# Optimization experiments

Measured on AMD Instinct MI355X. Metric: run time of the kernel, lower is better.

Reference implementation:

```python
import jax, jax.numpy as jnp
import numpy as np

B, S, F_IN = 8, 2048, 1024
H, SC = 512, 256
N_LAYERS = 3


def _glorot(key, shape):
    fan_in, fan_out = shape[-2], shape[-1]
    lim = float(np.sqrt(6.0 / (fan_in + fan_out)))
    return jax.random.uniform(key, shape, jnp.float32, -lim, lim)


def setup_inputs() -> dict:
    key = jax.random.key(0)
    ks = jax.random.split(key, 8)
    x = jax.random.normal(ks[0], (B, S, F_IN), jnp.float32)
    Wp = _glorot(ks[1], (F_IN, H)); bp = jnp.zeros((H,), jnp.float32)
    gcn_W = _glorot(ks[2], (N_LAYERS, H, H)); gcn_b = jnp.zeros((N_LAYERS, H), jnp.float32)
    s1_W = _glorot(ks[3], (H, SC)); s1_b = jnp.zeros((SC,), jnp.float32)
    s2_W = _glorot(ks[4], (SC, SC // 2)); s2_b = jnp.zeros((SC // 2,), jnp.float32)
    s3_W = _glorot(ks[5], (SC // 2, 1)); s3_b = jnp.zeros((1,), jnp.float32)
    return {"x": x, "Wp": Wp, "bp": bp, "gcn_W": gcn_W, "gcn_b": gcn_b,
            "s1_W": s1_W, "s1_b": s1_b, "s2_W": s2_W, "s2_b": s2_b,
            "s3_W": s3_W, "s3_b": s3_b}


def _build_adj(seq_len):
    # tridiagonal band: self + immediate temporal neighbors
    a = jnp.eye(seq_len, dtype=jnp.float32)
    a = a + jnp.eye(seq_len, k=1, dtype=jnp.float32) + jnp.eye(seq_len, k=-1, dtype=jnp.float32)
    deg = a.sum(axis=1)
    dinv = jnp.power(deg + 1e-8, -0.5)
    # D^{-1/2} A D^{-1/2}
    return dinv[:, None] * a * dinv[None, :]


def reference(x, Wp, bp, gcn_W, gcn_b, s1_W, s1_b, s2_W, s2_b, s3_W, s3_b):
    seq_len = x.shape[1]
    adj = _build_adj(seq_len)  # [S, S]
    h = jnp.einsum('bsf,fh->bsh', x, Wp) + bp  # feature projection
    for i in range(N_LAYERS):
        support = jnp.einsum('bsh,hk->bsk', h, gcn_W[i])
        h = jnp.einsum('st,btk->bsk', adj, support) + gcn_b[i]
        if i < N_LAYERS - 1:
            h = jax.nn.relu(h)  # dropout is identity in eval mode
    z = jax.nn.relu(jnp.einsum('bsh,hc->bsc', h, s1_W) + s1_b)
    z = jax.nn.relu(jnp.einsum('bsc,cd->bsd', z, s2_W) + s2_b)
    scores = jax.nn.sigmoid(jnp.einsum('bsd,do->bso', z, s3_W) + s3_b)
    return scores[..., 0]  # [B, S]
```

## Files before the change

kernel.cpp:

```cpp
#include <hip/hip_runtime.h>
#include <hip/hip_fp16.h>
#include <cstdint>
#include <cstddef>


typedef _Float16 f16;
typedef _Float16 f16x8 __attribute__((ext_vector_type(8)));
typedef float    f32x4 __attribute__((ext_vector_type(4)));

__device__ __forceinline__ void async_cp16(const void* g, void* l) {
  __builtin_amdgcn_global_load_lds((const __attribute__((address_space(1))) void*)g,
                                   (__attribute__((address_space(3))) void*)l, 16, 0, 0);
}

__device__ __forceinline__ f16x8 splat8(f16 v) {
  f16x8 r;
#pragma unroll
  for (int e = 0; e < 8; ++e) r[e] = v;
  return r;
}

template<int BM, int BN, bool RELU, bool HAS_BIAS, int AMODE>
__global__ __launch_bounds__(512, 4) void gemm_f16_kernel(
    const void* __restrict__ Aptr, const f16* __restrict__ BT,
    f16* __restrict__ C, const float* __restrict__ bias,
    int M, int N, int K)
{
  constexpr int BK = 64;
  constexpr int NT = 512;
  constexpr int WAVES_M = 2, WAVES_N = 4;
  constexpr int WM = BM / WAVES_M;
  constexpr int WN = BN / WAVES_N;
  constexpr int TM = WM / 16;
  constexpr int TN = WN / 16;
  constexpr int ITER_B = (BN * BK) / (NT * 8);
  constexpr int S = 2048;
  constexpr int AROWS = (AMODE == 2) ? (BM + 2) : BM;

  __shared__ __align__(16) f16 sA[AROWS * BK];
  __shared__ __align__(16) f16 sB[BN * BK];

  const int tid  = threadIdx.x;
  const int lane = tid & 63;
  const int wave = tid >> 6;
  const int wm   = wave / WAVES_N;
  const int wn   = wave % WAVES_N;
  const int m0   = blockIdx.x * BM;
  const int n0   = blockIdx.y * BN;
  const int quad = lane >> 4;
  const int l16  = lane & 15;

  const float dM = 0.57735026919f;
  const float dE = 0.70710678118f;

  f16 cf[TM][3];
  if constexpr (AMODE == 2) {
#pragma unroll
    for (int mi = 0; mi < TM; ++mi) {
      const int grow = m0 + wm * WM + mi * 16 + l16;
      const int s = grow & (S - 1);
      const float dsv = (s == 0 || s == S - 1) ? dE : dM;
      cf[mi][0] = (f16)((s > 0)     ? dsv * ((s - 1 == 0) ? dE : dM)     : 0.0f);
      cf[mi][1] = (f16)(dsv * dsv);
      cf[mi][2] = (f16)((s < S - 1) ? dsv * ((s + 1 == S - 1) ? dE : dM) : 0.0f);
    }
  }

  uint32_t offA = 0;
  {
    const int row = tid >> 3;
    const int q   = (tid & 7) ^ (row & 7);
    if constexpr (AMODE == 1)
      offA = (uint32_t)(((size_t)(m0 + row) * K + q * 8) * 4);
  }

  f32x4 acc[TM][TN];
#pragma unroll
  for (int i = 0; i < TM; ++i)
#pragma unroll
    for (int j = 0; j < TN; ++j)
      acc[i][j] = (f32x4){0.f, 0.f, 0.f, 0.f};

  float4 pa0, pa1;
  if constexpr (AMODE == 1) {
    const char* base = (const char*)Aptr;
    const float4* p = (const float4*)(base + offA);
    pa0 = p[0]; pa1 = p[1];
  }

  for (int kt = 0; kt < K; kt += BK) {
#pragma unroll
    for (int j = 0; j < ITER_B; ++j) {
      const int linear = j * NT + tid;
      const int row = linear >> 3;
      const int q   = (linear & 7) ^ (row & 7);
      async_cp16(BT + (size_t)(n0 + row) * K + kt + q * 8, &sB[linear * 8]);
    }
    if constexpr (AMODE == 1) {
      f16x8 o;
      o[0] = (f16)pa0.x; o[1] = (f16)pa0.y; o[2] = (f16)pa0.z; o[3] = (f16)pa0.w;
      o[4] = (f16)pa1.x; o[5] = (f16)pa1.y; o[6] = (f16)pa1.z; o[7] = (f16)pa1.w;
      *(f16x8*)&sA[(size_t)tid * 8] = o;
    } else {
      {
        const int chunk = tid + 8;
        const int row = chunk >> 3;
        const int q   = (chunk & 7) ^ (row & 7);
        async_cp16((const f16*)Aptr + (size_t)(m0 + row - 1) * K + kt + q * 8,
                   &sA[chunk * 8]);
      }
      if (tid < 16) {
        const int hi = tid >> 3;
        const int ldsrow = hi ? (BM + 1) : 0;
        const int i = tid & 7;
        const int q = i ^ (ldsrow & 7);
        int g = m0 - 1 + ldsrow;
        g = g < 0 ? 0 : (g >= M ? M - 1 : g);
        f16x8 v = *(const f16x8*)((const f16*)Aptr + (size_t)g * K + kt + q * 8);
        *(f16x8*)&sA[(size_t)(ldsrow * 8 + i) * 8] = v;
      }
    }
    __syncthreads();

    if constexpr (AMODE == 1) {
      if (kt + BK < K) {
        const char* base = (const char*)Aptr + (size_t)(kt + BK) * 4;
        const float4* p = (const float4*)(base + offA);
        pa0 = p[0]; pa1 = p[1];
      }
    }

#pragma unroll
    for (int kk = 0; kk < 2; ++kk) {
      const int c = quad + kk * 4;
      f16x8 af[TM], bf[TN];
#pragma unroll
      for (int mi = 0; mi < TM; ++mi) {
        if constexpr (AMODE == 2) {
          const int ldr = wm * WM + mi * 16 + l16 + 1;
          f16x8 pv = *(const f16x8*)&sA[(ldr - 1) * 64 + ((c ^ ((ldr - 1) & 7)) * 8)];
          f16x8 sv = *(const f16x8*)&sA[(ldr    ) * 64 + ((c ^ ((ldr    ) & 7)) * 8)];
          f16x8 nv = *(const f16x8*)&sA[(ldr + 1) * 64 + ((c ^ ((ldr + 1) & 7)) * 8)];
          f16x8 r = pv * splat8(cf[mi][0]);
          r += sv * splat8(cf[mi][1]);
          r += nv * splat8(cf[mi][2]);
          af[mi] = r;
        } else {
          const int ml = wm * WM + mi * 16 + l16;
          af[mi] = *(const f16x8*)&sA[ml * 64 + ((c ^ (ml & 7)) * 8)];
        }
      }
#pragma unroll
      for (int ni = 0; ni < TN; ++ni) {
        const int nl = wn * WN + ni * 16 + l16;
        bf[ni] = *(const f16x8*)&sB[nl * 64 + ((c ^ (nl & 7)) * 8)];
      }
#pragma unroll
      for (int mi = 0; mi < TM; ++mi)
#pragma unroll
        for (int ni = 0; ni < TN; ++ni)
          acc[mi][ni] = __builtin_amdgcn_mfma_f32_16x16x32_f16(
              af[mi], bf[ni], acc[mi][ni], 0, 0, 0);
    }
    __syncthreads();
  }

#pragma unroll
  for (int ni = 0; ni < TN; ++ni) {
    const int nc = n0 + wn * WN + ni * 16 + l16;
    const float bv = HAS_BIAS ? bias[nc] : 0.0f;
#pragma unroll
    for (int mi = 0; mi < TM; ++mi) {
#pragma unroll
      for (int r = 0; r < 4; ++r) {
        const int mr = m0 + wm * WM + mi * 16 + quad * 4 + r;
        float v = acc[mi][ni][r] + bv;
        if (RELU) v = fmaxf(v, 0.0f);
        C[(size_t)mr * N + nc] = (f16)v;
      }
    }
  }
}

__global__ __launch_bounds__(256) void head_fused_kernel(
    const f16* __restrict__ h, const f16* __restrict__ S1T,
    const f16* __restrict__ S2T,
    const float* __restrict__ s1b, const float* __restrict__ s2b,
    const float* __restrict__ s3w, const float* __restrict__ s3b,
    float* __restrict__ out)
{
  __shared__ __align__(16) char smem[36864 + 32 * 264 * 2];
  f16* sA  = (f16*)smem;
  f16* sB  = (f16*)(smem + 4096);
  f16* zs  = (f16*)(smem + 36864);
  f16* z2s = (f16*)smem;
  f16* sB2 = (f16*)(smem + 8704);

  const int tid  = threadIdx.x;
  const int lane = tid & 63;
  const int wave = tid >> 6;
  const int quad = lane >> 4;
  const int l16  = lane & 15;
  const int m0   = blockIdx.x * 32;

  f32x4 acc[2][4];
#pragma unroll
  for (int i = 0; i < 2; ++i)
#pragma unroll
    for (int j = 0; j < 4; ++j) acc[i][j] = (f32x4){0.f, 0.f, 0.f, 0.f};

  for (int kt = 0; kt < 512; kt += 64) {
    __syncthreads();
    {
      const int linear = tid;
      const int row = linear >> 3;
      const int q   = (linear & 7) ^ (row & 7);
      async_cp16(h + (size_t)(m0 + row) * 512 + kt + q * 8, &sA[linear * 8]);
    }
#pragma unroll
    for (int j = 0; j < 8; ++j) {
      const int linear = j * 256 + tid;
      const int row = linear >> 3;
      const int q   = (linear & 7) ^ (row & 7);
      async_cp16(S1T + (size_t)row * 512 + kt + q * 8, &sB[linear * 8]);
    }
    __syncthreads();
#pragma unroll
    for (int kk = 0; kk < 2; ++kk) {
      const int c = quad + kk * 4;
      f16x8 af[2], bf[4];
#pragma unroll
      for (int mi = 0; mi < 2; ++mi) {
        const int ml = mi * 16 + l16;
        af[mi] = *(const f16x8*)&sA[ml * 64 + ((c ^ (ml & 7)) * 8)];
      }
#pragma unroll
      for (int ni = 0; ni < 4; ++ni) {
        const int nl = wave * 64 + ni * 16 + l16;
        bf[ni] = *(const f16x8*)&sB[nl * 64 + ((c ^ (nl & 7)) * 8)];
      }
#pragma unroll
      for (int mi = 0; mi < 2; ++mi)
#pragma unroll
        for (int ni = 0; ni < 4; ++ni)
          acc[mi][ni] = __builtin_amdgcn_mfma_f32_16x16x32_f16(
              af[mi], bf[ni], acc[mi][ni], 0, 0, 0);
    }
  }
#pragma unroll
  for (int ni = 0; ni < 4; ++ni) {
    const int nc = wave * 64 + ni * 16 + l16;
    const float bv = s1b[nc];
#pragma unroll
    for (int mi = 0; mi < 2; ++mi)
#pragma unroll
      for (int r = 0; r < 4; ++r) {
        const int row = mi * 16 + quad * 4 + r;
        zs[row * 264 + nc] = (f16)fmaxf(acc[mi][ni][r] + bv, 0.0f);
      }
  }
  __syncthreads();

  f32x4 acc2[2][2];
#pragma unroll
  for (int i = 0; i < 2; ++i)
#pragma unroll
    for (int j = 0; j < 2; ++j) acc2[i][j] = (f32x4){0.f, 0.f, 0.f, 0.f};

  for (int kt2 = 0; kt2 < 4; ++kt2) {
    __syncthreads();
#pragma unroll
    for (int j = 0; j < 4; ++j) {
      const int linear = j * 256 + tid;
      const int row = linear >> 3;
      const int q   = (linear & 7) ^ (row & 7);
      async_cp16(S2T + (size_t)row * 256 + kt2 * 64 + q * 8, &sB2[linear * 8]);
    }
    __syncthreads();
#pragma unroll
    for (int kk = 0; kk < 2; ++kk) {
      const int c = quad + kk * 4;
      f16x8 af[2], bf[2];
#pragma unroll
      for (int mi = 0; mi < 2; ++mi) {
        const int row = mi * 16 + l16;
        af[mi] = *(const f16x8*)&zs[row * 264 + (kt2 * 8 + c) * 8];
      }
#pragma unroll
      for (int ni = 0; ni < 2; ++ni) {
        const int nl = wave * 32 + ni * 16 + l16;
        bf[ni] = *(const f16x8*)&sB2[nl * 64 + ((c ^ (nl & 7)) * 8)];
      }
#pragma unroll
      for (int mi = 0; mi < 2; ++mi)
#pragma unroll
        for (int ni = 0; ni < 2; ++ni)
          acc2[mi][ni] = __builtin_amdgcn_mfma_f32_16x16x32_f16(
              af[mi], bf[ni], acc2[mi][ni], 0, 0, 0);
    }
  }
  __syncthreads();
#pragma unroll
  for (int ni = 0; ni < 2; ++ni) {
    const int nc = wave * 32 + ni * 16 + l16;
    const float bv = s2b[nc];
#pragma unroll
    for (int mi = 0; mi < 2; ++mi)
#pragma unroll
      for (int r = 0; r < 4; ++r) {
        const int row = mi * 16 + quad * 4 + r;
        z2s[row * 136 + nc] = (f16)fmaxf(acc2[mi][ni][r] + bv, 0.0f);
      }
  }
  __syncthreads();

  const int m  = tid >> 3;
  const int qd = tid & 7;
  float p = 0.f;
#pragma unroll
  for (int j = 0; j < 2; ++j) {
    f16x8 v = *(const f16x8*)&z2s[m * 136 + qd * 16 + j * 8];
#pragma unroll
    for (int e = 0; e < 8; ++e) p += (float)v[e] * s3w[qd * 16 + j * 8 + e];
  }
  p += __shfl_xor(p, 1);
  p += __shfl_xor(p, 2);
  p += __shfl_xor(p, 4);
  if (qd == 0) out[m0 + m] = 1.0f / (1.0f + expf(-(p + s3b[0])));
}

__global__ __launch_bounds__(256) void prep_kernel(
    const float* __restrict__ Wp, f16* __restrict__ WpT,
    const float* __restrict__ gW, f16* __restrict__ GT,
    const float* __restrict__ s1W, f16* __restrict__ S1T,
    const float* __restrict__ s2W, f16* __restrict__ S2T)
{
  __shared__ f16 s[64 * 68];
  const int tid = threadIdx.x;
  int b = blockIdx.x;

  const float* W; f16* WT; int K, N, tile;
  if (b < 128)      { W = Wp;  WT = WpT; K = 1024; N = 512; tile = b; }
  else if (b < 320) { const int i = (b - 128) >> 6;
                      W = gW + (size_t)i * 262144; WT = GT + (size_t)i * 262144;
                      K = 512; N = 512; tile = (b - 128) & 63; }
  else if (b < 352) { W = s1W; WT = S1T; K = 512; N = 256; tile = b - 320; }
  else              { W = s2W; WT = S2T; K = 256; N = 128; tile = b - 352; }

  const int nt = tile % (N >> 6);
  const int kt = tile / (N >> 6);
#pragma unroll
  for (int it = 0; it < 16; ++it) {
    const int i  = it * 256 + tid;
    const int rk = i >> 6, rn = i & 63;
    s[rn * 68 + rk] = (f16)W[(size_t)(kt * 64 + rk) * N + nt * 64 + rn];
  }
  __syncthreads();
#pragma unroll
  for (int it = 0; it < 16; ++it) {
    const int i  = it * 256 + tid;
    const int rn = i >> 6, rk = i & 63;
    WT[(size_t)(nt * 64 + rn) * K + kt * 64 + rk] = s[rn * 68 + rk];
  }
}

extern "C" void kernel_launch(void* const* d_in, const int* in_sizes, int n_in,
                              void* d_out, int out_size, void* d_ws, size_t ws_size,
                              hipStream_t stream) {
  (void)in_sizes; (void)n_in; (void)out_size; (void)ws_size;
  const float* x   = (const float*)d_in[0];
  const float* Wp  = (const float*)d_in[1];
  const float* bp  = (const float*)d_in[2];
  const float* gW  = (const float*)d_in[3];
  const float* gb  = (const float*)d_in[4];
  const float* s1W = (const float*)d_in[5];
  const float* s1b = (const float*)d_in[6];
  const float* s2W = (const float*)d_in[7];
  const float* s2b = (const float*)d_in[8];
  const float* s3W = (const float*)d_in[9];
  const float* s3b = (const float*)d_in[10];
  float* out = (float*)d_out;

  constexpr int M = 16384;
  char* ws = (char*)d_ws;
  f16* hA  = (f16*)(ws + 0);
  f16* hB  = (f16*)(ws + 16777216);
  f16* WpT = (f16*)(ws + 33554432);
  f16* GT  = (f16*)(ws + 34603008);
  f16* S1T = (f16*)(ws + 36175872);
  f16* S2T = (f16*)(ws + 36438016);

  prep_kernel<<<360, 256, 0, stream>>>(Wp, WpT, gW, GT, s1W, S1T, s2W, S2T);

  gemm_f16_kernel<64, 256, false, true, 1>
      <<<dim3(M / 64, 2), 512, 0, stream>>>(x, WpT, hA, bp, M, 512, 1024);

  gemm_f16_kernel<64, 256, true, true, 2>
      <<<dim3(M / 64, 2), 512, 0, stream>>>(hA, GT, hB, gb, M, 512, 512);
  gemm_f16_kernel<64, 256, true, true, 2>
      <<<dim3(M / 64, 2), 512, 0, stream>>>(hB, GT + 262144, hA, gb + 512, M, 512, 512);
  gemm_f16_kernel<64, 256, false, true, 2>
      <<<dim3(M / 64, 2), 512, 0, stream>>>(hA, GT + 524288, hB, gb + 1024, M, 512, 512);

  head_fused_kernel<<<M / 32, 256, 0, stream>>>(hB, S1T, S2T, s1b, s2b, s3W, s3b, out);
}
```

Measured before the change: 198.2 us.

## Fuse three GCN layers into one kernel with LDS-resident activations and halo recompute

Replaces the three per-layer GEMM launches with one kernel. Each block loads a 96-row tile of h (64 output rows plus 16-row halos on each side) into LDS and runs all three layers in place, applying the tridiagonal stencil on the fly. This removes the global write and re-read of the intermediate activations between layers and two kernel launches. In exchange it recomputes the halo rows (1.5x the GEMM work), uses about 128KB of LDS so only one block fits per CU, and streams weights in small unpipelined K-steps with a barrier each step.

```diff
diff --git a/kernel.cpp b/kernel.cpp
--- a/kernel.cpp
+++ b/kernel.cpp
@@ -20,24 +20,22 @@
   return r;
 }
 
-template<int BM, int BN, bool RELU, bool HAS_BIAS, int AMODE>
-__global__ __launch_bounds__(512, 4) void gemm_f16_kernel(
-    const void* __restrict__ Aptr, const f16* __restrict__ BT,
+template<int BM, int BN, bool RELU, bool HAS_BIAS>
+__global__ __launch_bounds__(512, 4) void proj_gemm_kernel(
+    const float* __restrict__ Aptr, const f16* __restrict__ BT,
     f16* __restrict__ C, const float* __restrict__ bias,
     int M, int N, int K)
 {
   constexpr int BK = 64;
   constexpr int NT = 512;
-  constexpr int WAVES_M = 2, WAVES_N = 4;
-  constexpr int WM = BM / WAVES_M;
+  constexpr int WAVES_N = 4;
+  constexpr int WM = BM / 2;
   constexpr int WN = BN / WAVES_N;
   constexpr int TM = WM / 16;
   constexpr int TN = WN / 16;
   constexpr int ITER_B = (BN * BK) / (NT * 8);
-  constexpr int S = 2048;
-  constexpr int AROWS = (AMODE == 2) ? (BM + 2) : BM;
-
-  __shared__ __align__(16) f16 sA[AROWS * BK];
+
+  __shared__ __align__(16) f16 sA[BM * BK];
   __shared__ __align__(16) f16 sB[BN * BK];
 
   const int tid  = threadIdx.x;
@@ -50,28 +48,11 @@
   const int quad = lane >> 4;
   const int l16  = lane & 15;
 
-  const float dM = 0.57735026919f;
-  const float dE = 0.70710678118f;
-
-  f16 cf[TM][3];
-  if constexpr (AMODE == 2) {
-#pragma unroll
-    for (int mi = 0; mi < TM; ++mi) {
-      const int grow = m0 + wm * WM + mi * 16 + l16;
-      const int s = grow & (S - 1);
-      const float dsv = (s == 0 || s == S - 1) ? dE : dM;
-      cf[mi][0] = (f16)((s > 0)     ? dsv * ((s - 1 == 0) ? dE : dM)     : 0.0f);
-      cf[mi][1] = (f16)(dsv * dsv);
-      cf[mi][2] = (f16)((s < S - 1) ? dsv * ((s + 1 == S - 1) ? dE : dM) : 0.0f);
-    }
-  }
-
-  uint32_t offA = 0;
+  uint32_t offA;
   {
     const int row = tid >> 3;
     const int q   = (tid & 7) ^ (row & 7);
-    if constexpr (AMODE == 1)
-      offA = (uint32_t)(((size_t)(m0 + row) * K + q * 8) * 4);
+    offA = (uint32_t)(((size_t)(m0 + row) * K + q * 8) * 4);
   }
 
   f32x4 acc[TM][TN];
@@ -82,9 +63,8 @@
       acc[i][j] = (f32x4){0.f, 0.f, 0.f, 0.f};
 
   float4 pa0, pa1;
-  if constexpr (AMODE == 1) {
-    const char* base = (const char*)Aptr;
-    const float4* p = (const float4*)(base + offA);
+  {
+    const float4* p = (const float4*)((const char*)Aptr + offA);
     pa0 = p[0]; pa1 = p[1];
   }
 
@@ -96,38 +76,17 @@
       const int q   = (linear & 7) ^ (row & 7);
       async_cp16(BT + (size_t)(n0 + row) * K + kt + q * 8, &sB[linear * 8]);
     }
-    if constexpr (AMODE == 1) {
+    {
       f16x8 o;
       o[0] = (f16)pa0.x; o[1] = (f16)pa0.y; o[2] = (f16)pa0.z; o[3] = (f16)pa0.w;
       o[4] = (f16)pa1.x; o[5] = (f16)pa1.y; o[6] = (f16)pa1.z; o[7] = (f16)pa1.w;
       *(f16x8*)&sA[(size_t)tid * 8] = o;
-    } else {
-      {
-        const int chunk = tid + 8;
-        const int row = chunk >> 3;
-        const int q   = (chunk & 7) ^ (row & 7);
-        async_cp16((const f16*)Aptr + (size_t)(m0 + row - 1) * K + kt + q * 8,
-                   &sA[chunk * 8]);
-      }
-      if (tid < 16) {
-        const int hi = tid >> 3;
-        const int ldsrow = hi ? (BM + 1) : 0;
-        const int i = tid & 7;
-        const int q = i ^ (ldsrow & 7);
-        int g = m0 - 1 + ldsrow;
-        g = g < 0 ? 0 : (g >= M ? M - 1 : g);
-        f16x8 v = *(const f16x8*)((const f16*)Aptr + (size_t)g * K + kt + q * 8);
-        *(f16x8*)&sA[(size_t)(ldsrow * 8 + i) * 8] = v;
-      }
-    }
-    __syncthreads();
-
-    if constexpr (AMODE == 1) {
-      if (kt + BK < K) {
-        const char* base = (const char*)Aptr + (size_t)(kt + BK) * 4;
-        const float4* p = (const float4*)(base + offA);
-        pa0 = p[0]; pa1 = p[1];
-      }
+    }
+    __syncthreads();
+
+    if (kt + BK < K) {
+      const float4* p = (const float4*)((const char*)Aptr + (size_t)(kt + BK) * 4 + offA);
+      pa0 = p[0]; pa1 = p[1];
     }
 
 #pragma unroll
@@ -136,19 +95,8 @@
       f16x8 af[TM], bf[TN];
 #pragma unroll
       for (int mi = 0; mi < TM; ++mi) {
-        if constexpr (AMODE == 2) {
-          const int ldr = wm * WM + mi * 16 + l16 + 1;
-          f16x8 pv = *(const f16x8*)&sA[(ldr - 1) * 64 + ((c ^ ((ldr - 1) & 7)) * 8)];
-          f16x8 sv = *(const f16x8*)&sA[(ldr    ) * 64 + ((c ^ ((ldr    ) & 7)) * 8)];
-          f16x8 nv = *(const f16x8*)&sA[(ldr + 1) * 64 + ((c ^ ((ldr + 1) & 7)) * 8)];
-          f16x8 r = pv * splat8(cf[mi][0]);
-          r += sv * splat8(cf[mi][1]);
-          r += nv * splat8(cf[mi][2]);
-          af[mi] = r;
-        } else {
-          const int ml = wm * WM + mi * 16 + l16;
-          af[mi] = *(const f16x8*)&sA[ml * 64 + ((c ^ (ml & 7)) * 8)];
-        }
+        const int ml = wm * WM + mi * 16 + l16;
+        af[mi] = *(const f16x8*)&sA[ml * 64 + ((c ^ (ml & 7)) * 8)];
       }
 #pragma unroll
       for (int ni = 0; ni < TN; ++ni) {
@@ -177,6 +125,143 @@
         float v = acc[mi][ni][r] + bv;
         if (RELU) v = fmaxf(v, 0.0f);
         C[(size_t)mr * N + nc] = (f16)v;
+      }
+    }
+  }
+}
+
+__global__ __launch_bounds__(512, 2) void gcn_fused_kernel(
+    const f16* __restrict__ hin, const f16* __restrict__ GT,
+    const float* __restrict__ gb, f16* __restrict__ hout, int M)
+{
+  constexpr int ROWS = 96, HALO = 16, BK = 32, S = 2048;
+  constexpr int H = 512;
+  constexpr int TM = 3, TN = 8;
+
+  __shared__ __align__(16) f16 sh[ROWS * H];
+  __shared__ __align__(16) f16 sW[H * BK];
+
+  const int tid  = threadIdx.x;
+  const int lane = tid & 63;
+  const int wave = tid >> 6;
+  const int wm   = wave >> 2;
+  const int wn   = wave & 3;
+  const int quad = lane >> 4;
+  const int l16  = lane & 15;
+  const int m0   = blockIdx.x * 64;
+
+  const float dM = 0.57735026919f;
+  const float dE = 0.70710678118f;
+
+  f16 cf[TM][3];
+  int rS[TM], rP[TM], rN[TM];
+#pragma unroll
+  for (int mi = 0; mi < TM; ++mi) {
+    const int lr = wm * 48 + mi * 16 + l16;
+    const int g  = m0 - HALO + lr;
+    const int s  = g & (S - 1);
+    const float dsv = (s == 0 || s == S - 1) ? dE : dM;
+    cf[mi][0] = (f16)((s > 0)     ? dsv * ((s - 1 == 0) ? dE : dM)     : 0.0f);
+    cf[mi][1] = (f16)(dsv * dsv);
+    cf[mi][2] = (f16)((s < S - 1) ? dsv * ((s + 1 == S - 1) ? dE : dM) : 0.0f);
+    rS[mi] = lr;
+    rP[mi] = (lr > 0)        ? lr - 1 : 0;
+    rN[mi] = (lr < ROWS - 1) ? lr + 1 : ROWS-1;
+  }
+
+#pragma unroll
+  for (int j = 0; j < 12; ++j) {
+    const int row = j * 8 + wave;
+    const int q   = lane ^ (row & 7) ^ (lane & ~63);
+    const int cin = lane;
+    const int qq  = cin ^ (row & 7);
+    int g = m0 - HALO + row;
+    g = g < 0 ? 0 : (g >= M ? M - 1 : g);
+    (void)q;
+    async_cp16(hin + (size_t)g * H + qq * 8, &sh[((size_t)j * 512 + tid) * 8]);
+  }
+
+  for (int L = 0; L < 3; ++L) {
+    const f16* WL = GT + (size_t)L * 262144;
+    const float* bL = gb + L * 512;
+
+    f32x4 acc[TM][TN];
+#pragma unroll
+    for (int i = 0; i < TM; ++i)
+#pragma unroll
+      for (int j = 0; j < TN; ++j)
+        acc[i][j] = (f32x4){0.f, 0.f, 0.f, 0.f};
+
+    for (int kt = 0; kt < H; kt += BK) {
+#pragma unroll
+      for (int j = 0; j < 4; ++j) {
+        const int linear = j * 512 + tid;
+        const int row = linear >> 2;
+        const int cin = linear & 3;
+        const int qq  = cin ^ (row & 3);
+        async_cp16(WL + (size_t)row * H + kt + qq * 8, &sW[(size_t)linear * 8]);
+      }
+      __syncthreads();
+
+      const int cb = kt >> 3;
+      f16x8 af[TM], bf[TN];
+#pragma unroll
+      for (int mi = 0; mi < TM; ++mi) {
+        const int c = cb + quad;
+        f16x8 pv = *(const f16x8*)&sh[rP[mi] * H + ((c ^ (rP[mi] & 7)) * 8)];
+        f16x8 sv = *(const f16x8*)&sh[rS[mi] * H + ((c ^ (rS[mi] & 7)) * 8)];
+        f16x8 nv = *(const f16x8*)&sh[rN[mi] * H + ((c ^ (rN[mi] & 7)) * 8)];
+        f16x8 r = pv * splat8(cf[mi][0]);
+        r += sv * splat8(cf[mi][1]);
+        r += nv * splat8(cf[mi][2]);
+        af[mi] = r;
+      }
+#pragma unroll
+      for (int ni = 0; ni < TN; ++ni) {
+        const int nl = wn * 128 + ni * 16 + l16;
+        bf[ni] = *(const f16x8*)&sW[nl * BK + ((quad ^ (nl & 3)) * 8)];
+      }
+#pragma unroll
+      for (int mi = 0; mi < TM; ++mi)
+#pragma unroll
+        for (int ni = 0; ni < TN; ++ni)
+          acc[mi][ni] = __builtin_amdgcn_mfma_f32_16x16x32_f16(
+              af[mi], bf[ni], acc[mi][ni], 0, 0, 0);
+      __syncthreads();
+    }
+
+    if (L < 2) {
+#pragma unroll
+      for (int ni = 0; ni < TN; ++ni) {
+        const int nc = wn * 128 + ni * 16 + l16;
+        const int chunk = nc >> 3;
+        const float bv = bL[nc];
+#pragma unroll
+        for (int mi = 0; mi < TM; ++mi) {
+#pragma unroll
+          for (int r = 0; r < 4; ++r) {
+            const int row = wm * 48 + mi * 16 + quad * 4 + r;
+            const float v = fmaxf(acc[mi][ni][r] + bv, 0.0f);
+            sh[row * H + ((chunk ^ (row & 7)) * 8) + (nc & 7)] = (f16)v;
+          }
+        }
+      }
+    } else {
+#pragma unroll
+      for (int ni = 0; ni < TN; ++ni) {
+        const int nc = wn * 128 + ni * 16 + l16;
+        const float bv = bL[nc];
+#pragma unroll
+        for (int mi = 0; mi < TM; ++mi) {
+#pragma unroll
+          for (int r = 0; r < 4; ++r) {
+            const int lr = wm * 48 + mi * 16 + quad * 4 + r;
+            if (lr >= HALO && lr < HALO + 64) {
+              const float v = acc[mi][ni][r] + bv;
+              hout[(size_t)(m0 + lr - HALO) * H + nc] = (f16)v;
+            }
+          }
+        }
       }
     }
   }
@@ -392,15 +477,10 @@
 
   prep_kernel<<<360, 256, 0, stream>>>(Wp, WpT, gW, GT, s1W, S1T, s2W, S2T);
 
-  gemm_f16_kernel<64, 256, false, true, 1>
+  proj_gemm_kernel<64, 256, false, true>
       <<<dim3(M / 64, 2), 512, 0, stream>>>(x, WpT, hA, bp, M, 512, 1024);
 
-  gemm_f16_kernel<64, 256, true, true, 2>
-      <<<dim3(M / 64, 2), 512, 0, stream>>>(hA, GT, hB, gb, M, 512, 512);
-  gemm_f16_kernel<64, 256, true, true, 2>
-      <<<dim3(M / 64, 2), 512, 0, stream>>>(hB, GT + 262144, hA, gb + 512, M, 512, 512);
-  gemm_f16_kernel<64, 256, false, true, 2>
-      <<<dim3(M / 64, 2), 512, 0, stream>>>(hA, GT + 524288, hB, gb + 1024, M, 512, 512);
+  gcn_fused_kernel<<<M / 64, 512, 0, stream>>>(hA, GT, gb, hB, M);
 
   head_fused_kernel<<<M / 32, 256, 0, stream>>>(hB, S1T, S2T, s1b, s2b, s3W, s3b, out);
 }
```

Result: slower. 272.9 us (+37.7%).
